# Kernel optimization log

Hardware: AMD Instinct MI355X
Metric: run time of the kernel (lower is better)

Reference implementation:

```python
import jax, jax.numpy as jnp
import numpy as np

SEQ_LEN = 1024
D_MODEL = 512
K_FILT = 24
HEADS = 8
R = 512  # must equal d_model for the module's forward to type-check
NFFT = 2048  # nearest power of two >= 2*SEQ_LEN-1
LN_EPS = 1e-5


def _spectral_filters():
    # Hankel matrix Z[i,j] = 2 / ((i+j)^3 - (i+j)), i,j in 1..T
    e = np.arange(1, SEQ_LEN + 1, dtype=np.float64)
    ipj = e[:, None] + e[None, :]
    Z = 2.0 / (ipj ** 3 - ipj)
    sigma, phi = np.linalg.eigh(Z)
    sigma_k = np.clip(sigma[-K_FILT:], 1e-9, None)
    phi_k = phi[:, -K_FILT:] * sigma_k ** 0.25
    return phi_k.astype(np.float32)  # (T, K)


def setup_inputs() -> dict:
    key = jax.random.key(0)
    ks = jax.random.split(key, 12)
    s = 0.02
    B = 2

    def lin(k):
        kw, kb = jax.random.split(k)
        return (jax.random.normal(kw, (D_MODEL, D_MODEL), jnp.float32) * s,
                jax.random.normal(kb, (D_MODEL,), jnp.float32) * s)

    Wq, bq = lin(ks[0]); Wk, bk = lin(ks[1]); Wv, bv = lin(ks[2])
    Wg, bg = lin(ks[3]); Wo, bo = lin(ks[4])
    return {
        'x': jax.random.normal(ks[5], (B, SEQ_LEN, D_MODEL), jnp.float32),
        'stu_filters': jnp.asarray(_spectral_filters()),
        'M_inputs': jax.random.normal(ks[6], (D_MODEL, R), jnp.float32) * s,
        'M_filters': jax.random.normal(ks[7], (K_FILT, R), jnp.float32) * s,
        'Wq': Wq, 'bq': bq, 'Wk': Wk, 'bk': bk, 'Wv': Wv, 'bv': bv,
        'Wg': Wg, 'bg': bg, 'Wo': Wo, 'bo': bo,
        'ln_w': jnp.ones((R,), jnp.float32),
        'ln_b': jnp.zeros((R,), jnp.float32),
    }


def _stu_conv(u, v):
    # u: (B, T, r), v: (T, r). FFT-based causal conv with sign featurization.
    T = u.shape[1]
    sgn = jnp.where(jnp.arange(T) % 2 == 1, -1.0, 1.0)[None, :, None]  # (1,T,1)
    Vf = jnp.fft.rfft(v[None, :, :, None], n=NFFT, axis=1)  # (1,F,r,1)
    U = jnp.stack([u, u * sgn], axis=-1)  # (B,T,r,2)
    Uf = jnp.fft.rfft(U, n=NFFT, axis=1)  # (B,F,r,2)
    conv = jnp.fft.irfft(Vf * Uf, n=NFFT, axis=1)[:, :T]  # (B,T,r,2)
    return conv[..., 0], conv[..., 1] * sgn


def _layernorm(x, w, b):
    mu = jnp.mean(x, axis=-1, keepdims=True)
    var = jnp.mean((x - mu) ** 2, axis=-1, keepdims=True)
    return (x - mu) * jax.lax.rsqrt(var + LN_EPS) * w + b


def reference(x, stu_filters, M_inputs, M_filters, Wq, bq, Wk, bk, Wv, bv,
              Wg, bg, Wo, bo, ln_w, ln_b):
    B, T, d = x.shape
    hd = d // HEADS
    # STU features
    u_proj = x @ M_inputs                    # (B,T,r)
    phi_proj = stu_filters @ M_filters       # (T,r)
    sp, sm = _stu_conv(u_proj, phi_proj)
    x_tilde = _layernorm(sp + sm, ln_w, ln_b)  # (B,T,r==d)
    # gated linear attention with gelu features and causal cumsum state
    def proj(W, b):
        y = (x @ W.T + b).reshape(B, T, HEADS, hd).transpose(0, 2, 1, 3)
        return jax.nn.gelu(y, approximate=True)
    Q = proj(Wq, bq); K = proj(Wk, bk); V = proj(Wv, bv)
    Zt = jnp.einsum('bhtp,bhtn->bhtpn', V, K)   # (B,H,T,hd,hd)
    Hc = jnp.cumsum(Zt, axis=2)
    Y = jnp.einsum('bhtp,bhtpn->bhtn', Q, Hc)   # (B,H,T,hd)
    Y_attn = Y.transpose(0, 2, 1, 3).reshape(B, T, d)
    gate = jax.nn.sigmoid(x @ Wg.T + bg)
    comb = gate * Y_attn + (1.0 - gate) * x_tilde
    return comb @ Wo.T + bo
```

## Files before the change

kernel.cpp:

```cpp
#include <hip/hip_runtime.h>
#include <hip/hip_bf16.h>

#define T_SEQ 1024
#define D_MOD 512
#define NHEAD 8
#define HDIM  64
#define R_DIM 512
#define BATCH 2

typedef __attribute__((ext_vector_type(8))) __bf16 bf16x8;
typedef __attribute__((ext_vector_type(4))) float f32x4;

__device__ __forceinline__ float ldin(const void* p, size_t i, int bf) {
    if (bf) return __bfloat162float(((const __hip_bfloat16*)p)[i]);
    return ((const float*)p)[i];
}
__device__ __forceinline__ void stout(void* p, size_t i, int bf, float v) {
    if (bf) ((__hip_bfloat16*)p)[i] = __float2bfloat16(v);
    else    ((float*)p)[i] = v;
}

__device__ __forceinline__ float gelu_f(float x) {
    return 0.5f * x * (1.f + tanhf(0.7978845608028654f * (x + 0.044715f * x * x * x)));
}

__device__ __forceinline__ bf16x8 cvt8(float4 a, float4 b) {
    bf16x8 t;
    t[0]=(__bf16)a.x; t[1]=(__bf16)a.y; t[2]=(__bf16)a.z; t[3]=(__bf16)a.w;
    t[4]=(__bf16)b.x; t[5]=(__bf16)b.y; t[6]=(__bf16)b.z; t[7]=(__bf16)b.w;
    return t;
}

__device__ __forceinline__ int detect_bf(const void* x) {
    __shared__ int cnt;
    if (threadIdx.x == 0) cnt = 0;
    __syncthreads();
    const unsigned short* h = (const unsigned short*)x;
    int c = 0;
    for (int i = threadIdx.x; i < 8192; i += 256)
        if ((h[i] & 0x7F80u) == 0x7F80u) c++;
    if (c) atomicAdd(&cnt, c);
    __syncthreads();
    return cnt == 0;
}

__global__ __launch_bounds__(256) void mega_gemm(
    const void* __restrict__ x, const void* __restrict__ Mi,
    const void* __restrict__ stf, const void* __restrict__ Mf,
    const void* __restrict__ Wq, const void* __restrict__ bq,
    const void* __restrict__ Wk, const void* __restrict__ bk,
    const void* __restrict__ Wv, const void* __restrict__ bv,
    const void* __restrict__ Wg, const void* __restrict__ bg,
    float* __restrict__ fu, float* __restrict__ fphi,
    __bf16* __restrict__ fQ, __bf16* __restrict__ fKT,
    __bf16* __restrict__ fV, __bf16* __restrict__ fG)
{
    const int tid = threadIdx.x;
    const int job = blockIdx.z;
    if (job == 6) {
        float4* zp = (float4*)(fphi + 524288);
        const int bid = blockIdx.y * 8 + blockIdx.x;
        const float4 z4 = make_float4(0.f, 0.f, 0.f, 0.f);
        #pragma unroll
        for (int q = 0; q < 8; ++q)
            zp[(size_t)bid * 2048 + q * 256 + tid] = z4;
        return;
    }
    const int bf = detect_bf(x);
    const void* A = x; const void* Bw; const void* bias = nullptr;
    int Kd = 512, act = 0; bool trb = true;
    switch (job) {
        case 0: Bw = Mi; trb = false; break;
        case 1: Bw = Wq; bias = bq; act = 1; break;
        case 2: Bw = Wk; bias = bk; act = 1; break;
        case 3: Bw = Wv; bias = bv; act = 1; break;
        case 4: Bw = Wg; bias = bg; act = 2; break;
        default: A = stf; Bw = Mf; trb = false; Kd = 32; break;
    }
    const int M = (job == 5) ? 1024 : 2048;
    const int m0 = blockIdx.y * 64;
    if (m0 >= M) return;
    const int n0 = blockIdx.x * 64;

    __shared__ __align__(16) __bf16 sm[2][2 * 64 * 40];
    const int wave = tid >> 6, lane = tid & 63;
    const int lm = lane & 15, kq = lane >> 4;
    const int mo = tid >> 2, ko = (tid & 3) * 8;
    const int gn = tid & 63, gk = (tid >> 6) * 8;

    bf16x8 ba, bb;
    float4 fa0, fa1, fb0, fb1;

    auto issue = [&](int k0) {
        if (job == 5) {
            bf16x8 t;
            #pragma unroll
            for (int q = 0; q < 8; ++q) {
                const int k = ko + q;
                t[q] = (k < 24) ? (__bf16)ldin(A, (size_t)(m0 + mo) * 24 + k, bf)
                                : (__bf16)0.f;
            }
            ba = t;
        } else if (bf) {
            ba = *(const bf16x8*)((const __bf16*)A + (size_t)(m0 + mo) * 512 + k0 + ko);
        } else {
            const float* Af = (const float*)A + (size_t)(m0 + mo) * 512 + k0 + ko;
            fa0 = *(const float4*)Af; fa1 = *(const float4*)(Af + 4);
        }
        if (trb) {
            const size_t go = (size_t)(n0 + mo) * 512 + k0 + ko;
            if (bf) {
                bb = *(const bf16x8*)((const __bf16*)Bw + go);
            } else {
                const float* Bf = (const float*)Bw + go;
                fb0 = *(const float4*)Bf; fb1 = *(const float4*)(Bf + 4);
            }
        } else {
            bf16x8 t;
            #pragma unroll
            for (int e = 0; e < 8; ++e) {
                const int k = k0 + gk + e;
                t[e] = (job == 5 && k >= 24) ? (__bf16)0.f
                     : (__bf16)ldin(Bw, (size_t)k * 512 + n0 + gn, bf);
            }
            bb = t;
        }
    };
    auto commit = [&](int bi) {
        __bf16 (*As)[40] = (__bf16 (*)[40])sm[bi];
        __bf16 (*Bs)[40] = (__bf16 (*)[40])(sm[bi] + 64 * 40);
        bf16x8 va = ba, vb = bb;
        if (job != 5 && !bf) va = cvt8(fa0, fa1);
        if (trb && !bf)      vb = cvt8(fb0, fb1);
        *(bf16x8*)&As[mo][ko] = va;
        if (trb) *(bf16x8*)&Bs[mo][ko] = vb;
        else     *(bf16x8*)&Bs[gn][gk] = vb;
    };

    f32x4 acc[4] = {};
    issue(0);
    commit(0);
    __syncthreads();
    int cur = 0;
    for (int k0 = 0; k0 < Kd; k0 += 32) {
        const bool haveNext = (k0 + 32 < Kd);
        if (haveNext) issue(k0 + 32);
        __bf16 (*As)[40] = (__bf16 (*)[40])sm[cur];
        __bf16 (*Bs)[40] = (__bf16 (*)[40])(sm[cur] + 64 * 40);
        const bf16x8 a = *(const bf16x8*)&As[wave * 16 + lm][kq * 8];
        #pragma unroll
        for (int nt = 0; nt < 4; ++nt) {
            const bf16x8 b = *(const bf16x8*)&Bs[nt * 16 + lm][kq * 8];
            acc[nt] = __builtin_amdgcn_mfma_f32_16x16x32_bf16(a, b, acc[nt], 0, 0, 0);
        }
        if (haveNext) {
            commit(cur ^ 1);
            __syncthreads();
            cur ^= 1;
        }
    }
    if (job == 2) {
        __syncthreads();
        __bf16 (*Kt)[72] = (__bf16 (*)[72])sm[0];
        #pragma unroll
        for (int nt = 0; nt < 4; ++nt) {
            const int n = nt * 16 + lm;
            #pragma unroll
            for (int r2 = 0; r2 < 4; ++r2) {
                float v = acc[nt][r2] + ldin(bias, (size_t)(n0 + n), bf);
                Kt[n][wave * 16 + kq * 4 + r2] = (__bf16)gelu_f(v);
            }
        }
        __syncthreads();
        const int h = n0 >> 6;
        const int b = m0 >> 10;
        const int tb = m0 & 1023;
        #pragma unroll
        for (int q = 0; q < 2; ++q) {
            const int c = q * 256 + tid;
            const int p = c >> 3, off = (c & 7) * 8;
            *(bf16x8*)&fKT[(((size_t)b * NHEAD + h) * 64 + p) * T_SEQ + tb + off] =
                *(const bf16x8*)&Kt[p][off];
        }
        return;
    }
    #pragma unroll
    for (int nt = 0; nt < 4; ++nt) {
        const int n = n0 + nt * 16 + lm;
        #pragma unroll
        for (int r2 = 0; r2 < 4; ++r2) {
            const int m = m0 + wave * 16 + kq * 4 + r2;
            float v = acc[nt][r2];
            if (bias) v += ldin(bias, (size_t)n, bf);
            if (act == 1) v = gelu_f(v);
            if (act == 2) v = 1.f / (1.f + expf(-v));
            switch (job) {
                case 0: fu[(size_t)m * 512 + n] = v; break;
                case 5: fphi[(size_t)m * 512 + n] = v; break;
                case 1: fQ[(size_t)m * 512 + n] = (__bf16)v; break;
                case 3: fV[(size_t)m * 512 + n] = (__bf16)v; break;
                default: fG[(size_t)m * 512 + n] = (__bf16)v; break;
            }
        }
    }
}

__global__ __launch_bounds__(256) void conv_attn_k(
    const float* __restrict__ u, const float* __restrict__ vphi,
    float* __restrict__ w,
    const __bf16* __restrict__ Q, const __bf16* __restrict__ KT,
    const __bf16* __restrict__ V, float* __restrict__ Y)
{
    __shared__ __align__(16) unsigned char smem[49152];
    const int tid = threadIdx.x;
    const int z = blockIdx.z;
    int rem = blockIdx.x, ti = 0;
    while (rem >= ((ti + 4) >> 2)) { rem -= (ti + 4) >> 2; ++ti; }
    const int jlo = rem * 4;
    const int jhi = (jlo + 3 < ti) ? jlo + 3 : ti;
    const int t0 = ti * 64;

    if (z < 2) {
        float (*vs)[64] = (float (*)[64])smem;
        float (*us)[64] = (float (*)[64])(smem + 16384);
        const int rl = tid & 63, tg = tid >> 6;
        const int b = z;
        const int r0 = blockIdx.y * 64;
        const float* ub = u + (size_t)b * T_SEQ * R_DIM;
        float acc[16] = {};
        for (int j = jlo; j <= jhi; ++j) {
            if (j != jlo) __syncthreads();
            const int L0 = j * 64;
            const int W0 = t0 - L0 - 63;
            #pragma unroll
            for (int jj = 0; jj < 8; ++jj) {
                const int n = jj * 256 + tid;
                const int row = n >> 4, c4 = (n & 15) * 4;
                int s = W0 + row;
                s = s < 0 ? 0 : (s > T_SEQ - 1 ? T_SEQ - 1 : s);
                *(float4*)&us[row][c4] = *(const float4*)&ub[(size_t)s * R_DIM + r0 + c4];
            }
            #pragma unroll
            for (int jj = 0; jj < 4; ++jj) {
                const int n = jj * 256 + tid;
                const int row = n >> 4, c4 = (n & 15) * 4;
                *(float4*)&vs[row][c4] = *(const float4*)&vphi[(size_t)(L0 + row) * R_DIM + r0 + c4];
            }
            __syncthreads();
            if (j < ti) {
                #pragma unroll
                for (int g = 0; g < 4; ++g) {
                    const int wsmin = tg * 16 + 49 - 16 * g;
                    float ur[30];
                    #pragma unroll
                    for (int q = 0; q < 30; ++q) ur[q] = us[wsmin + q][rl];
                    float vr[8];
                    #pragma unroll
                    for (int e = 0; e < 8; ++e) vr[e] = vs[16 * g + 2 * e][rl];
                    #pragma unroll
                    for (int e = 0; e < 8; ++e)
                        #pragma unroll
                        for (int i = 0; i < 16; ++i)
                            acc[i] += vr[e] * ur[i - 2 * e + 14];
                }
            } else {
                for (int l = 0; l < 64; l += 2) {
                    const float vv = vs[l][rl];
                    #pragma unroll
                    for (int i = 0; i < 16; ++i) {
                        const int srel = tg * 16 + i - l;
                        if (srel >= 0) acc[i] += vv * us[srel + 63][rl];
                    }
                }
            }
        }
        #pragma unroll
        for (int i = 0; i < 16; ++i)
            atomicAdd(&w[((size_t)b * T_SEQ + t0 + tg * 16 + i) * R_DIM + r0 + rl],
                      2.f * acc[i]);
    } else {
        __bf16 (*Qs)[72] = (__bf16 (*)[72])smem;
        __bf16 (*Vs)[72] = (__bf16 (*)[72])(smem + 9216);
        __bf16 (*Kt)[72] = (__bf16 (*)[72])(smem + 18432);
        __bf16 (*Sa)[72] = (__bf16 (*)[72])(smem + 27648);
        const int wave = tid >> 6, lane = tid & 63;
        const int lm = lane & 15, kq = lane >> 4;
        const int b = z - 2;
        const int h = blockIdx.y;
        const size_t cbase = ((size_t)b * T_SEQ) * D_MOD + h * HDIM;
        const __bf16* KTh = KT + (((size_t)b * NHEAD + h) * 64) * T_SEQ;
        #pragma unroll
        for (int it = 0; it < 2; ++it) {
            const int n = it * 256 + tid;
            const int row = n >> 3, p0 = (n & 7) * 8;
            *(bf16x8*)&Qs[row][p0] = *(const bf16x8*)&Q[cbase + (size_t)(t0 + row) * D_MOD + p0];
        }
        f32x4 accY[4] = {};
        for (int j = jlo; j <= jhi; ++j) {
            const int s0 = j * 64;
            __syncthreads();
            #pragma unroll
            for (int it = 0; it < 2; ++it) {
                const int n = it * 256 + tid;
                const int row = n >> 3, c0 = (n & 7) * 8;
                *(bf16x8*)&Vs[row][c0] = *(const bf16x8*)&V[cbase + (size_t)(s0 + row) * D_MOD + c0];
                *(bf16x8*)&Kt[row][c0] = *(const bf16x8*)&KTh[(size_t)row * T_SEQ + s0 + c0];
            }
            __syncthreads();
            f32x4 sacc[4] = {};
            #pragma unroll
            for (int ks = 0; ks < 2; ++ks) {
                const bf16x8 a = *(const bf16x8*)&Qs[wave * 16 + lm][ks * 32 + kq * 8];
                #pragma unroll
                for (int nt = 0; nt < 4; ++nt) {
                    const bf16x8 bb = *(const bf16x8*)&Vs[nt * 16 + lm][ks * 32 + kq * 8];
                    sacc[nt] = __builtin_amdgcn_mfma_f32_16x16x32_bf16(a, bb, sacc[nt], 0, 0, 0);
                }
            }
            const bool diag = (j == ti);
            #pragma unroll
            for (int nt = 0; nt < 4; ++nt) {
                const int sl = nt * 16 + lm;
                #pragma unroll
                for (int r2 = 0; r2 < 4; ++r2) {
                    const int tl = wave * 16 + kq * 4 + r2;
                    float v = sacc[nt][r2];
                    if (diag && sl > tl) v = 0.f;
                    Sa[tl][sl] = (__bf16)v;
                }
            }
            #pragma unroll
            for (int ks = 0; ks < 2; ++ks) {
                const bf16x8 a = *(const bf16x8*)&Sa[wave * 16 + lm][ks * 32 + kq * 8];
                #pragma unroll
                for (int nt = 0; nt < 4; ++nt) {
                    const bf16x8 bb = *(const bf16x8*)&Kt[nt * 16 + lm][ks * 32 + kq * 8];
                    accY[nt] = __builtin_amdgcn_mfma_f32_16x16x32_bf16(a, bb, accY[nt], 0, 0, 0);
                }
            }
        }
        #pragma unroll
        for (int nt = 0; nt < 4; ++nt) {
            const int nh = nt * 16 + lm;
            #pragma unroll
            for (int r2 = 0; r2 < 4; ++r2) {
                const int tl = wave * 16 + kq * 4 + r2;
                atomicAdd(&Y[cbase + (size_t)(t0 + tl) * D_MOD + nh], accY[nt][r2]);
            }
        }
    }
}

__global__ __launch_bounds__(256) void ln_k(float* __restrict__ w,
                                            const void* __restrict__ g,
                                            const void* __restrict__ b,
                                            const void* __restrict__ xref)
{
    const int bf = detect_bf(xref);
    const size_t row = (size_t)blockIdx.y * T_SEQ + blockIdx.x;
    float* p = w + row * R_DIM;
    const int tid = threadIdx.x;
    const float x0 = p[tid], x1 = p[tid + 256];
    __shared__ float red[4];
    float s = x0 + x1;
    #pragma unroll
    for (int off = 32; off > 0; off >>= 1) s += __shfl_down(s, off, 64);
    if ((tid & 63) == 0) red[tid >> 6] = s;
    __syncthreads();
    const float mu = (red[0] + red[1] + red[2] + red[3]) * (1.f / 512.f);
    __syncthreads();
    const float d0 = x0 - mu, d1 = x1 - mu;
    float vsum = d0 * d0 + d1 * d1;
    #pragma unroll
    for (int off = 32; off > 0; off >>= 1) vsum += __shfl_down(vsum, off, 64);
    if ((tid & 63) == 0) red[tid >> 6] = vsum;
    __syncthreads();
    const float var = (red[0] + red[1] + red[2] + red[3]) * (1.f / 512.f);
    const float rs = rsqrtf(var + 1e-5f);
    p[tid]       = d0 * rs * ldin(g, tid, bf)       + ldin(b, tid, bf);
    p[tid + 256] = d1 * rs * ldin(g, tid + 256, bf) + ldin(b, tid + 256, bf);
}

__global__ __launch_bounds__(256) void final_gemm(const __bf16* __restrict__ G,
                                                  const float* __restrict__ Yf,
                                                  const float* __restrict__ Xt,
                                                  const void* __restrict__ Wo,
                                                  const void* __restrict__ bo,
                                                  void* __restrict__ out,
                                                  const void* __restrict__ xref)
{
    const int bf = detect_bf(xref);
    __shared__ __align__(16) __bf16 sm[2][2 * 64 * 40];
    const int tid = threadIdx.x;
    const int wave = tid >> 6, lane = tid & 63;
    const int lm = lane & 15, kq = lane >> 4;
    const int mo = tid >> 2, ko = (tid & 3) * 8;
    const int m0 = blockIdx.y * 64, n0 = blockIdx.x * 64;

    bf16x8 pg, pw;
    float4 py0, py1, px0, px1, pw0, pw1;

    auto issue = [&](int k0) {
        const size_t off = (size_t)(m0 + mo) * 512 + k0 + ko;
        pg  = *(const bf16x8*)(G + off);
        py0 = *(const float4*)(Yf + off); py1 = *(const float4*)(Yf + off + 4);
        px0 = *(const float4*)(Xt + off); px1 = *(const float4*)(Xt + off + 4);
        const size_t ob = (size_t)(n0 + mo) * 512 + k0 + ko;
        if (bf) pw = *(const bf16x8*)((const __bf16*)Wo + ob);
        else { const float* Bf = (const float*)Wo + ob;
               pw0 = *(const float4*)Bf; pw1 = *(const float4*)(Bf + 4); }
    };
    auto commit = [&](int bi) {
        __bf16 (*As)[40] = (__bf16 (*)[40])sm[bi];
        __bf16 (*Bs)[40] = (__bf16 (*)[40])(sm[bi] + 64 * 40);
        const float yv[8] = {py0.x,py0.y,py0.z,py0.w,py1.x,py1.y,py1.z,py1.w};
        const float xv[8] = {px0.x,px0.y,px0.z,px0.w,px1.x,px1.y,px1.z,px1.w};
        bf16x8 t;
        #pragma unroll
        for (int q = 0; q < 8; ++q) {
            const float gg = (float)pg[q];
            t[q] = (__bf16)(gg * yv[q] + (1.f - gg) * xv[q]);
        }
        *(bf16x8*)&As[mo][ko] = t;
        *(bf16x8*)&Bs[mo][ko] = bf ? pw : cvt8(pw0, pw1);
    };

    f32x4 acc[4] = {};
    issue(0);
    commit(0);
    __syncthreads();
    int cur = 0;
    for (int k0 = 0; k0 < 512; k0 += 32) {
        const bool haveNext = (k0 + 32 < 512);
        if (haveNext) issue(k0 + 32);
        __bf16 (*As)[40] = (__bf16 (*)[40])sm[cur];
        __bf16 (*Bs)[40] = (__bf16 (*)[40])(sm[cur] + 64 * 40);
        const bf16x8 a = *(const bf16x8*)&As[wave * 16 + lm][kq * 8];
        #pragma unroll
        for (int nt = 0; nt < 4; ++nt) {
            const bf16x8 b = *(const bf16x8*)&Bs[nt * 16 + lm][kq * 8];
            acc[nt] = __builtin_amdgcn_mfma_f32_16x16x32_bf16(a, b, acc[nt], 0, 0, 0);
        }
        if (haveNext) {
            commit(cur ^ 1);
            __syncthreads();
            cur ^= 1;
        }
    }
    #pragma unroll
    for (int nt = 0; nt < 4; ++nt) {
        const int n = n0 + nt * 16 + lm;
        #pragma unroll
        for (int r2 = 0; r2 < 4; ++r2) {
            const int m = m0 + wave * 16 + kq * 4 + r2;
            float v = acc[nt][r2] + ldin(bo, (size_t)n, bf);
            stout(out, (size_t)m * 512 + n, bf, v);
        }
    }
}

extern "C" void kernel_launch(void* const* d_in, const int* in_sizes, int n_in,
                              void* d_out, int out_size, void* d_ws, size_t ws_size,
                              hipStream_t stream)
{
    const void* x   = d_in[0];
    const void* stf = d_in[1];
    const void* Mi  = d_in[2];
    const void* Mf  = d_in[3];
    const void* Wq  = d_in[4];  const void* bq = d_in[5];
    const void* Wk  = d_in[6];  const void* bk = d_in[7];
    const void* Wv  = d_in[8];  const void* bv = d_in[9];
    const void* Wg  = d_in[10]; const void* bg = d_in[11];
    const void* Wo  = d_in[12]; const void* bo = d_in[13];
    const void* lnw = d_in[14]; const void* lnb = d_in[15];

    float* base = (float*)d_ws;
    float*  f_u   = base;
    float*  f_phi = base + 1048576;
    float*  f_w   = base + 1572864;
    float*  f_Y   = base + 2621440;
    __bf16* f_Q   = (__bf16*)(base + 3670016);
    __bf16* f_KT  = f_Q + 1048576;
    __bf16* f_V   = f_KT + 1048576;
    __bf16* f_G   = f_V + 1048576;

    dim3 blk(256);

    mega_gemm<<<dim3(8, 32, 7), blk, 0, stream>>>(
        x, Mi, stf, Mf, Wq, bq, Wk, bk, Wv, bv, Wg, bg,
        f_u, f_phi, f_Q, f_KT, f_V, f_G);

    conv_attn_k<<<dim3(40, 8, 4), blk, 0, stream>>>(f_u, f_phi, f_w, f_Q, f_KT, f_V, f_Y);

    ln_k<<<dim3(T_SEQ, BATCH), blk, 0, stream>>>(f_w, lnw, lnb, x);

    final_gemm<<<dim3(8, 32), blk, 0, stream>>>(f_G, f_Y, f_w, Wo, bo, d_out, x);
}
```

Before: 202.4 us.

## Store STU projections in bf16 and simplify the fused GEMM staging

```diff
diff --git a/kernel.cpp b/kernel.cpp
--- a/kernel.cpp
+++ b/kernel.cpp
@@ -9,6 +9,7 @@
 #define BATCH 2
 
 typedef __attribute__((ext_vector_type(8))) __bf16 bf16x8;
+typedef __attribute__((ext_vector_type(4))) __bf16 bf16x4;
 typedef __attribute__((ext_vector_type(4))) float f32x4;
 
 __device__ __forceinline__ float ldin(const void* p, size_t i, int bf) {
@@ -51,7 +52,7 @@
     const void* __restrict__ Wk, const void* __restrict__ bk,
     const void* __restrict__ Wv, const void* __restrict__ bv,
     const void* __restrict__ Wg, const void* __restrict__ bg,
-    float* __restrict__ fu, float* __restrict__ fphi,
+    __bf16* __restrict__ fu, __bf16* __restrict__ fphi,
     __bf16* __restrict__ fQ, __bf16* __restrict__ fKT,
     __bf16* __restrict__ fV, __bf16* __restrict__ fG)
 {
@@ -82,107 +83,71 @@
     if (m0 >= M) return;
     const int n0 = blockIdx.x * 64;
 
-    __shared__ __align__(16) __bf16 sm[2][2 * 64 * 40];
+    __shared__ __align__(16) __bf16 As[64][40];
+    __shared__ __align__(16) __bf16 Bs[64][40];
     const int wave = tid >> 6, lane = tid & 63;
     const int lm = lane & 15, kq = lane >> 4;
-    const int mo = tid >> 2, ko = (tid & 3) * 8;
-    const int gn = tid & 63, gk = (tid >> 6) * 8;
-
-    bf16x8 ba, bb;
-    float4 fa0, fa1, fb0, fb1;
-
-    auto issue = [&](int k0) {
-        if (job == 5) {
-            bf16x8 t;
-            #pragma unroll
-            for (int q = 0; q < 8; ++q) {
-                const int k = ko + q;
-                t[q] = (k < 24) ? (__bf16)ldin(A, (size_t)(m0 + mo) * 24 + k, bf)
-                                : (__bf16)0.f;
-            }
-            ba = t;
-        } else if (bf) {
-            ba = *(const bf16x8*)((const __bf16*)A + (size_t)(m0 + mo) * 512 + k0 + ko);
-        } else {
-            const float* Af = (const float*)A + (size_t)(m0 + mo) * 512 + k0 + ko;
-            fa0 = *(const float4*)Af; fa1 = *(const float4*)(Af + 4);
+
+    f32x4 acc[4] = {};
+
+    for (int k0 = 0; k0 < Kd; k0 += 32) {
+        if (k0) __syncthreads();
+        {
+            const int mo = tid >> 2;
+            const int ko = (tid & 3) * 8;
+            if (job == 5) {
+                #pragma unroll
+                for (int q = 0; q < 8; ++q) {
+                    const int k = ko + q;
+                    As[mo][k] = (k < 24) ? (__bf16)ldin(A, (size_t)(m0 + mo) * 24 + k, bf)
+                                         : (__bf16)0.f;
+                }
+            } else if (bf) {
+                *(bf16x8*)&As[mo][ko] =
+                    *(const bf16x8*)((const __bf16*)A + (size_t)(m0 + mo) * 512 + k0 + ko);
+            } else {
+                const float* Af = (const float*)A + (size_t)(m0 + mo) * 512 + k0 + ko;
+                *(bf16x8*)&As[mo][ko] = cvt8(*(const float4*)Af, *(const float4*)(Af + 4));
+            }
         }
         if (trb) {
-            const size_t go = (size_t)(n0 + mo) * 512 + k0 + ko;
+            const int no = tid >> 2;
+            const int ko = (tid & 3) * 8;
+            const size_t go = (size_t)(n0 + no) * 512 + k0 + ko;
             if (bf) {
-                bb = *(const bf16x8*)((const __bf16*)Bw + go);
+                *(bf16x8*)&Bs[no][ko] = *(const bf16x8*)((const __bf16*)Bw + go);
             } else {
                 const float* Bf = (const float*)Bw + go;
-                fb0 = *(const float4*)Bf; fb1 = *(const float4*)(Bf + 4);
+                *(bf16x8*)&Bs[no][ko] = cvt8(*(const float4*)Bf, *(const float4*)(Bf + 4));
             }
         } else {
-            bf16x8 t;
-            #pragma unroll
-            for (int e = 0; e < 8; ++e) {
-                const int k = k0 + gk + e;
-                t[e] = (job == 5 && k >= 24) ? (__bf16)0.f
-                     : (__bf16)ldin(Bw, (size_t)k * 512 + n0 + gn, bf);
-            }
-            bb = t;
-        }
-    };
-    auto commit = [&](int bi) {
-        __bf16 (*As)[40] = (__bf16 (*)[40])sm[bi];
-        __bf16 (*Bs)[40] = (__bf16 (*)[40])(sm[bi] + 64 * 40);
-        bf16x8 va = ba, vb = bb;
-        if (job != 5 && !bf) va = cvt8(fa0, fa1);
-        if (trb && !bf)      vb = cvt8(fb0, fb1);
-        *(bf16x8*)&As[mo][ko] = va;
-        if (trb) *(bf16x8*)&Bs[mo][ko] = vb;
-        else     *(bf16x8*)&Bs[gn][gk] = vb;
-    };
-
-    f32x4 acc[4] = {};
-    issue(0);
-    commit(0);
-    __syncthreads();
-    int cur = 0;
-    for (int k0 = 0; k0 < Kd; k0 += 32) {
-        const bool haveNext = (k0 + 32 < Kd);
-        if (haveNext) issue(k0 + 32);
-        __bf16 (*As)[40] = (__bf16 (*)[40])sm[cur];
-        __bf16 (*Bs)[40] = (__bf16 (*)[40])(sm[cur] + 64 * 40);
+            const int kk = tid >> 3;
+            const int nn = (tid & 7) * 8;
+            if (job == 5) {
+                #pragma unroll
+                for (int q = 0; q < 8; ++q)
+                    Bs[nn + q][kk] = (kk < 24) ? (__bf16)ldin(Bw, (size_t)kk * 512 + n0 + nn + q, bf)
+                                               : (__bf16)0.f;
+            } else {
+                const size_t off = (size_t)(k0 + kk) * 512 + n0 + nn;
+                if (bf) {
+                    const bf16x8 t = *(const bf16x8*)((const __bf16*)Bw + off);
+                    #pragma unroll
+                    for (int q = 0; q < 8; ++q) Bs[nn + q][kk] = t[q];
+                } else {
+                    const float* Bf = (const float*)Bw + off;
+                    #pragma unroll
+                    for (int q = 0; q < 8; ++q) Bs[nn + q][kk] = (__bf16)Bf[q];
+                }
+            }
+        }
+        __syncthreads();
         const bf16x8 a = *(const bf16x8*)&As[wave * 16 + lm][kq * 8];
         #pragma unroll
         for (int nt = 0; nt < 4; ++nt) {
             const bf16x8 b = *(const bf16x8*)&Bs[nt * 16 + lm][kq * 8];
             acc[nt] = __builtin_amdgcn_mfma_f32_16x16x32_bf16(a, b, acc[nt], 0, 0, 0);
         }
-        if (haveNext) {
-            commit(cur ^ 1);
-            __syncthreads();
-            cur ^= 1;
-        }
-    }
-    if (job == 2) {
-        __syncthreads();
-        __bf16 (*Kt)[72] = (__bf16 (*)[72])sm[0];
-        #pragma unroll
-        for (int nt = 0; nt < 4; ++nt) {
-            const int n = nt * 16 + lm;
-            #pragma unroll
-            for (int r2 = 0; r2 < 4; ++r2) {
-                float v = acc[nt][r2] + ldin(bias, (size_t)(n0 + n), bf);
-                Kt[n][wave * 16 + kq * 4 + r2] = (__bf16)gelu_f(v);
-            }
-        }
-        __syncthreads();
-        const int h = n0 >> 6;
-        const int b = m0 >> 10;
-        const int tb = m0 & 1023;
-        #pragma unroll
-        for (int q = 0; q < 2; ++q) {
-            const int c = q * 256 + tid;
-            const int p = c >> 3, off = (c & 7) * 8;
-            *(bf16x8*)&fKT[(((size_t)b * NHEAD + h) * 64 + p) * T_SEQ + tb + off] =
-                *(const bf16x8*)&Kt[p][off];
-        }
-        return;
     }
     #pragma unroll
     for (int nt = 0; nt < 4; ++nt) {
@@ -195,18 +160,24 @@
             if (act == 1) v = gelu_f(v);
             if (act == 2) v = 1.f / (1.f + expf(-v));
             switch (job) {
-                case 0: fu[(size_t)m * 512 + n] = v; break;
-                case 5: fphi[(size_t)m * 512 + n] = v; break;
+                case 0: fu[(size_t)m * 512 + n] = (__bf16)v; break;
+                case 5: fphi[(size_t)m * 512 + n] = (__bf16)v; break;
                 case 1: fQ[(size_t)m * 512 + n] = (__bf16)v; break;
                 case 3: fV[(size_t)m * 512 + n] = (__bf16)v; break;
-                default: fG[(size_t)m * 512 + n] = (__bf16)v; break;
+                case 4: fG[(size_t)m * 512 + n] = (__bf16)v; break;
+                case 2: {
+                    const int b = m >> 10, t = m & 1023;
+                    const int h = n >> 6,  p = n & 63;
+                    fKT[(((size_t)b * NHEAD + h) * 64 + p) * T_SEQ + t] = (__bf16)v;
+                    break;
+                }
             }
         }
     }
 }
 
 __global__ __launch_bounds__(256) void conv_attn_k(
-    const float* __restrict__ u, const float* __restrict__ vphi,
+    const __bf16* __restrict__ u, const __bf16* __restrict__ vphi,
     float* __restrict__ w,
     const __bf16* __restrict__ Q, const __bf16* __restrict__ KT,
     const __bf16* __restrict__ V, float* __restrict__ Y)
@@ -226,7 +197,7 @@
         const int rl = tid & 63, tg = tid >> 6;
         const int b = z;
         const int r0 = blockIdx.y * 64;
-        const float* ub = u + (size_t)b * T_SEQ * R_DIM;
+        const __bf16* ub = u + (size_t)b * T_SEQ * R_DIM;
         float acc[16] = {};
         for (int j = jlo; j <= jhi; ++j) {
             if (j != jlo) __syncthreads();
@@ -238,13 +209,17 @@
                 const int row = n >> 4, c4 = (n & 15) * 4;
                 int s = W0 + row;
                 s = s < 0 ? 0 : (s > T_SEQ - 1 ? T_SEQ - 1 : s);
-                *(float4*)&us[row][c4] = *(const float4*)&ub[(size_t)s * R_DIM + r0 + c4];
+                const bf16x4 t = *(const bf16x4*)&ub[(size_t)s * R_DIM + r0 + c4];
+                *(float4*)&us[row][c4] =
+                    make_float4((float)t[0], (float)t[1], (float)t[2], (float)t[3]);
             }
             #pragma unroll
             for (int jj = 0; jj < 4; ++jj) {
                 const int n = jj * 256 + tid;
                 const int row = n >> 4, c4 = (n & 15) * 4;
-                *(float4*)&vs[row][c4] = *(const float4*)&vphi[(size_t)(L0 + row) * R_DIM + r0 + c4];
+                const bf16x4 t = *(const bf16x4*)&vphi[(size_t)(L0 + row) * R_DIM + r0 + c4];
+                *(float4*)&vs[row][c4] =
+                    make_float4((float)t[0], (float)t[1], (float)t[2], (float)t[3]);
             }
             __syncthreads();
             if (j < ti) {
@@ -475,11 +450,11 @@
     const void* lnw = d_in[14]; const void* lnb = d_in[15];
 
     float* base = (float*)d_ws;
-    float*  f_u   = base;
-    float*  f_phi = base + 1048576;
-    float*  f_w   = base + 1572864;
-    float*  f_Y   = base + 2621440;
-    __bf16* f_Q   = (__bf16*)(base + 3670016);
+    __bf16* f_u   = (__bf16*)base;
+    __bf16* f_phi = f_u + 1048576;
+    float*  f_w   = base + 786432;
+    float*  f_Y   = base + 1835008;
+    __bf16* f_Q   = (__bf16*)(base + 2883584);
     __bf16* f_KT  = f_Q + 1048576;
     __bf16* f_V   = f_KT + 1048576;
     __bf16* f_G   = f_V + 1048576;
```

Result: faster. 186.2 us (-8.0%).
